# Kernel tuning notes

Hardware: AMD Instinct MI355X
Metric: run time of the kernel (lower is better)

The kernel has to match this reference:

```python
import jax, jax.numpy as jnp
import numpy as np

NUM_EMBEDDINGS = 1024
EMBEDDING_DIM = 256
COMMITMENT_COST = 0.25
DECAY = 0.99
EPS = 1e-5


def setup_inputs() -> dict:
    key = jax.random.key(0)
    k0, k1, k2 = jax.random.split(key, 3)
    x = jax.random.normal(k0, (32, 2048, EMBEDDING_DIM), dtype=jnp.float32)
    # embedding.weight.data.uniform_(-1/K, 1/K)
    embedding_w = jax.random.uniform(
        k1, (NUM_EMBEDDINGS, EMBEDDING_DIM), dtype=jnp.float32,
        minval=-1.0 / NUM_EMBEDDINGS, maxval=1.0 / NUM_EMBEDDINGS)
    ema_cluster_size = jnp.zeros((NUM_EMBEDDINGS,), dtype=jnp.float32)
    ema_w = jax.random.normal(k2, (NUM_EMBEDDINGS, EMBEDDING_DIM), dtype=jnp.float32)
    return {"x": x, "embedding_w": embedding_w,
            "ema_cluster_size": ema_cluster_size, "ema_w": ema_w}


def reference(x, embedding_w, ema_cluster_size, ema_w):
    K, D = embedding_w.shape
    flat = x.reshape(-1, D)  # [N, D]

    # squared L2 distances to codebook: [N, K]
    distances = ((flat * flat).sum(axis=1, keepdims=True)
                 - 2.0 * flat @ embedding_w.T
                 + (embedding_w * embedding_w).sum(axis=1))
    indices = jnp.argmin(distances, axis=1)  # [N] int

    # gather quantized vectors
    quantized = embedding_w[indices].reshape(x.shape)

    # EMA statistics via scatter-add (one-hot.T @ flat without materializing one-hot)
    counts = jax.ops.segment_sum(jnp.ones((flat.shape[0],), dtype=flat.dtype),
                                 indices, num_segments=K)  # [K]
    dw = jax.ops.segment_sum(flat, indices, num_segments=K)  # [K, D]

    new_cluster_size = DECAY * ema_cluster_size + (1.0 - DECAY) * counts
    new_ema_w = DECAY * ema_w + (1.0 - DECAY) * dw

    # Laplace smoothing of cluster sizes, normalized codebook update
    n = new_cluster_size.sum()
    cs = (new_cluster_size + EPS) / (n + K * EPS) * n
    new_embedding_w = new_ema_w / cs[:, None]

    # commitment loss (codebook side is EMA-updated, so only e-latent term)
    e_latent_loss = jnp.mean((jax.lax.stop_gradient(quantized) - x) ** 2)
    loss = COMMITMENT_COST * e_latent_loss

    # straight-through estimator
    quantized_st = x + jax.lax.stop_gradient(quantized - x)

    avg_probs = counts / counts.sum()
    perplexity = jnp.exp(-jnp.sum(avg_probs * jnp.log(avg_probs + 1e-10)))

    return (loss, quantized_st, perplexity,
            new_embedding_w, new_cluster_size, new_ema_w)
```

## Files before the change

kernel.cpp:

```cpp
#include <hip/hip_runtime.h>
#include <math.h>

#define N_ROWS   65536
#define K_EMB    1024
#define D_EMB    256

typedef __attribute__((ext_vector_type(8)))  short short8;
typedef __attribute__((ext_vector_type(4)))  short short4v;
typedef __attribute__((ext_vector_type(16))) float floatx16;

__device__ inline unsigned short f2bf(float f) {
    unsigned u = __float_as_uint(f);
    unsigned r = u + 0x7fffu + ((u >> 16) & 1u);
    return (unsigned short)(r >> 16);
}
__device__ inline float bf2f(unsigned short s) {
    return __uint_as_float(((unsigned)s) << 16);
}

__global__ __launch_bounds__(64)
void prep_e(const float* __restrict__ ew, float* __restrict__ half_esq,
            short* __restrict__ pack_hi, short* __restrict__ pack_lo,
            double* __restrict__ loss_buckets)
{
    const int k = blockIdx.x;
    const int t = threadIdx.x;

    if (t == 0 && k < 256) loss_buckets[k] = 0.0;

    float4 v = *(const float4*)(ew + (size_t)k * D_EMB + t * 4);
    float s = v.x * v.x + v.y * v.y + v.z * v.z + v.w * v.w;
#pragma unroll
    for (int off = 32; off > 0; off >>= 1) s += __shfl_down(s, off);
    if (t == 0) half_esq[k] = 0.5f * s;

    const int d0   = t * 4;
    const int tile = k >> 5;
    const int kt   = d0 >> 4;
    const int half = (d0 & 15) >> 3;
    const int lane = (k & 31) + 32 * half;
    const int j0   = d0 & 7;
    const int off  = tile * 8192 + kt * 512 + lane * 8 + j0;

    float f[4] = {-v.x, -v.y, -v.z, -v.w};
    short4v h, l;
#pragma unroll
    for (int j = 0; j < 4; ++j) {
        unsigned short hh = f2bf(f[j]);
        h[j] = (short)hh;
        l[j] = (short)f2bf(f[j] - bf2f(hh));
    }
    *(short4v*)(pack_hi + off) = h;
    *(short4v*)(pack_lo + off) = l;
}

__global__ __launch_bounds__(256, 2)
void argmin_mfma(const float* __restrict__ x,
                 const short* __restrict__ pack_hi,
                 const short* __restrict__ pack_lo,
                 const float* __restrict__ half_esq,
                 const float* __restrict__ ew,
                 int* __restrict__ indices,
                 float* __restrict__ out_q,
                 double* __restrict__ loss_buckets)
{
    __shared__ short xs_hi[32 * 256];
    __shared__ short xs_lo[32 * 256];
    __shared__ float cmv[128];
    __shared__ int   cmi[128];
    __shared__ int   widx[32];

    const int t  = threadIdx.x;
    const int r0 = blockIdx.x * 32;

#pragma unroll
    for (int i = 0; i < 4; ++i) {
        int q   = i * 256 + t;
        int row = q >> 5;
        int g8  = q & 31;
        const float* gp = x + (size_t)(r0 + row) * D_EMB + g8 * 8;
        float4 a = *(const float4*)gp;
        float4 b = *(const float4*)(gp + 4);
        float f[8] = {a.x, a.y, a.z, a.w, b.x, b.y, b.z, b.w};
        short8 h8, l8;
#pragma unroll
        for (int j = 0; j < 8; ++j) {
            unsigned short hh = f2bf(f[j]);
            h8[j] = (short)hh;
            l8[j] = (short)f2bf(f[j] - bf2f(hh));
        }
        int off = row * 256 + ((g8 ^ (row & 7)) << 3);
        *(short8*)(xs_hi + off) = h8;
        *(short8*)(xs_lo + off) = l8;
    }
    __syncthreads();

    const int w    = t >> 6;
    const int lane = t & 63;
    const int l31  = lane & 31;
    const int half = lane >> 5;
    const int key  = l31 & 7;
    const short* bbase_h = xs_hi + l31 * 256;
    const short* bbase_l = xs_lo + l31 * 256;

    float mv = 3.4e38f;
    int   mi = 0;

    for (int cp = 0; cp < 4; ++cp) {
        const int c0 = w * 256 + cp * 64;
        const int c1 = c0 + 32;
        const int tile0 = c0 >> 5;

        floatx16 acc0, acc1;
#pragma unroll
        for (int rq = 0; rq < 4; ++rq) {
            float4 e0 = *(const float4*)(half_esq + c0 + rq * 8 + half * 4);
            float4 e1 = *(const float4*)(half_esq + c1 + rq * 8 + half * 4);
            acc0[rq * 4 + 0] = e0.x; acc0[rq * 4 + 1] = e0.y;
            acc0[rq * 4 + 2] = e0.z; acc0[rq * 4 + 3] = e0.w;
            acc1[rq * 4 + 0] = e1.x; acc1[rq * 4 + 1] = e1.y;
            acc1[rq * 4 + 2] = e1.z; acc1[rq * 4 + 3] = e1.w;
        }

        const short* p0h = pack_hi + tile0 * 8192 + lane * 8;
        const short* p0l = pack_lo + tile0 * 8192 + lane * 8;
        const short* p1h = p0h + 8192;
        const short* p1l = p0l + 8192;

        short8 a0h = *(const short8*)(p0h);
        short8 a0l = *(const short8*)(p0l);
        short8 a1h = *(const short8*)(p1h);
        short8 a1l = *(const short8*)(p1l);

#pragma unroll 4
        for (int kt = 0; kt < 16; ++kt) {
            short8 n0h, n0l, n1h, n1l;
            if (kt < 15) {
                n0h = *(const short8*)(p0h + (kt + 1) * 512);
                n0l = *(const short8*)(p0l + (kt + 1) * 512);
                n1h = *(const short8*)(p1h + (kt + 1) * 512);
                n1l = *(const short8*)(p1l + (kt + 1) * 512);
            }
            int coff = (((2 * kt + half) ^ key) << 3);
            short8 bh = *(const short8*)(bbase_h + coff);
            short8 bl = *(const short8*)(bbase_l + coff);
            acc0 = __builtin_amdgcn_mfma_f32_32x32x16_bf16(a0h, bh, acc0, 0, 0, 0);
            acc1 = __builtin_amdgcn_mfma_f32_32x32x16_bf16(a1h, bh, acc1, 0, 0, 0);
            acc0 = __builtin_amdgcn_mfma_f32_32x32x16_bf16(a0h, bl, acc0, 0, 0, 0);
            acc1 = __builtin_amdgcn_mfma_f32_32x32x16_bf16(a1h, bl, acc1, 0, 0, 0);
            acc0 = __builtin_amdgcn_mfma_f32_32x32x16_bf16(a0l, bh, acc0, 0, 0, 0);
            acc1 = __builtin_amdgcn_mfma_f32_32x32x16_bf16(a1l, bh, acc1, 0, 0, 0);
            a0h = n0h; a0l = n0l; a1h = n1h; a1l = n1l;
        }

#pragma unroll
        for (int r = 0; r < 16; ++r) {
            int code0 = c0 + (r & 3) + ((r >> 2) << 3) + half * 4;
            float v0 = acc0[r];
            if (v0 < mv || (v0 == mv && code0 < mi)) { mv = v0; mi = code0; }
            int code1 = code0 + 32;
            float v1 = acc1[r];
            if (v1 < mv || (v1 == mv && code1 < mi)) { mv = v1; mi = code1; }
        }
    }

    {
        float ov = __shfl_xor(mv, 32);
        int   oi = __shfl_xor(mi, 32);
        if (ov < mv || (ov == mv && oi < mi)) { mv = ov; mi = oi; }
    }

    if (half == 0) {
        int slot = w * 32 + l31;
        cmv[slot] = mv;
        cmi[slot] = mi;
    }
    __syncthreads();
    if (t < 32) {
        float bv = cmv[t];
        int   bi = cmi[t];
#pragma unroll
        for (int ww = 1; ww < 4; ++ww) {
            float v = cmv[ww * 32 + t];
            int   i = cmi[ww * 32 + t];
            if (v < bv || (v == bv && i < bi)) { bv = v; bi = i; }
        }
        indices[r0 + t] = bi;
        widx[t] = bi;
    }
    __syncthreads();

    const int g8e  = lane >> 1;
    const int j0e  = (lane & 1) * 4;
    float lsum = 0.0f;
#pragma unroll
    for (int rr = 0; rr < 8; ++rr) {
        const int row = w * 8 + rr;
        const int idx = widx[row];
        const int off = row * 256 + (((g8e) ^ (row & 7)) << 3) + j0e;
        short4v h4 = *(const short4v*)(xs_hi + off);
        short4v l4 = *(const short4v*)(xs_lo + off);
        float xr[4];
#pragma unroll
        for (int j = 0; j < 4; ++j)
            xr[j] = bf2f((unsigned short)h4[j]) + bf2f((unsigned short)l4[j]);
        const float4 ev = *(const float4*)(ew + (size_t)idx * D_EMB + lane * 4);
        float4 q;
        q.x = xr[0] + (ev.x - xr[0]);
        q.y = xr[1] + (ev.y - xr[1]);
        q.z = xr[2] + (ev.z - xr[2]);
        q.w = xr[3] + (ev.w - xr[3]);
        *(float4*)(out_q + (size_t)(r0 + row) * D_EMB + lane * 4) = q;
        float dx = ev.x - xr[0], dy = ev.y - xr[1];
        float dz = ev.z - xr[2], dwv = ev.w - xr[3];
        lsum += dx * dx + dy * dy + dz * dz + dwv * dwv;
    }
#pragma unroll
    for (int off = 32; off > 0; off >>= 1) lsum += __shfl_down(lsum, off);
    if (lane == 0) atomicAdd(&loss_buckets[blockIdx.x & 255], (double)lsum);
}

__global__ __launch_bounds__(1024)
void finalize_small(const float* __restrict__ ema_cs,
                    const int* __restrict__ indices,
                    const double* __restrict__ loss_buckets,
                    float* __restrict__ cs_ws,
                    float* __restrict__ out_loss,
                    float* __restrict__ out_perp,
                    float* __restrict__ out_ncs,
                    int* __restrict__ counts,
                    int* __restrict__ offsets,
                    int* __restrict__ cursor)
{
    __shared__ int    hist[1024];
    __shared__ float  red[1024];
    __shared__ double redd[256];
    __shared__ int    sc[1024];
    const int k = threadIdx.x;

    hist[k] = 0;
    __syncthreads();
#pragma unroll
    for (int i = 0; i < 16; ++i) {
        int4 v = *(const int4*)(indices + (i * 1024 + k) * 4);
        atomicAdd(&hist[v.x], 1); atomicAdd(&hist[v.y], 1);
        atomicAdd(&hist[v.z], 1); atomicAdd(&hist[v.w], 1);
    }
    __syncthreads();

    const int icnt = hist[k];
    counts[k] = icnt;
    cursor[k] = 0;

    const float cnt = (float)icnt;
    const float ncs = 0.99f * ema_cs[k] + 0.01f * cnt;
    out_ncs[k] = ncs;
    red[k] = ncs;
    sc[k]  = icnt;
    __syncthreads();
    for (int off = 512; off > 0; off >>= 1) {
        if (k < off) red[k] += red[k + off];
        __syncthreads();
    }
    const float n = red[0];
    __syncthreads();
    cs_ws[k] = (ncs + 1e-5f) / (n + 1024.0f * 1e-5f) * n;

    for (int d = 1; d < 1024; d <<= 1) {
        int add = (k >= d) ? sc[k - d] : 0;
        __syncthreads();
        sc[k] += add;
        __syncthreads();
    }
    offsets[k] = sc[k] - icnt;

    const float p = cnt / 65536.0f;
    red[k] = p * logf(p + 1e-10f);
    if (k < 256) redd[k] = loss_buckets[k];
    __syncthreads();
    for (int off = 512; off > 0; off >>= 1) {
        if (k < off) red[k] += red[k + off];
        __syncthreads();
    }
    if (k == 0) out_perp[0] = expf(-red[0]);
    for (int off = 128; off > 0; off >>= 1) {
        if (k < off) redd[k] += redd[k + off];
        __syncthreads();
    }
    if (k == 0) out_loss[0] = (float)(0.25 * (redd[0] / 16777216.0));
}

__global__ __launch_bounds__(256)
void scatter_rows(const int* __restrict__ indices,
                  const int* __restrict__ offsets,
                  int* __restrict__ cursor,
                  int* __restrict__ row_sorted)
{
    const int row = blockIdx.x * 256 + threadIdx.x;
    const int idx = indices[row];
    const int pos = atomicAdd(&cursor[idx], 1);
    row_sorted[offsets[idx] + pos] = row;
}

__global__ __launch_bounds__(256)
void gather_update(const float* __restrict__ x,
                   const int* __restrict__ row_sorted,
                   const int* __restrict__ offsets,
                   const int* __restrict__ counts,
                   const float* __restrict__ ema_w,
                   const float* __restrict__ cs_ws,
                   float* __restrict__ out_emb,
                   float* __restrict__ out_ema)
{
    __shared__ int rows[2048];
    const int k   = blockIdx.x;
    const int t   = threadIdx.x;
    const int off = offsets[k];
    const int cnt = counts[k];
    float sum = 0.0f;

    for (int c = 0; c < cnt; c += 2048) {
        const int m = min(cnt - c, 2048);
        for (int i = t; i < m; i += 256) rows[i] = row_sorted[off + c + i];
        __syncthreads();
        int r = 0;
        for (; r + 4 <= m; r += 4) {
            int i0 = rows[r], i1 = rows[r + 1], i2 = rows[r + 2], i3 = rows[r + 3];
            float v0 = x[(size_t)i0 * D_EMB + t];
            float v1 = x[(size_t)i1 * D_EMB + t];
            float v2 = x[(size_t)i2 * D_EMB + t];
            float v3 = x[(size_t)i3 * D_EMB + t];
            sum += (v0 + v1) + (v2 + v3);
        }
        for (; r < m; ++r)
            sum += x[(size_t)rows[r] * D_EMB + t];
        __syncthreads();
    }

    const size_t o = (size_t)k * D_EMB + t;
    const float nev = 0.99f * ema_w[o] + 0.01f * sum;
    out_ema[o] = nev;
    out_emb[o] = nev / cs_ws[k];
}

extern "C" void kernel_launch(void* const* d_in, const int* in_sizes, int n_in,
                              void* d_out, int out_size, void* d_ws, size_t ws_size,
                              hipStream_t stream)
{
    const float* x       = (const float*)d_in[0];
    const float* ew      = (const float*)d_in[1];
    const float* ema_cs  = (const float*)d_in[2];
    const float* ema_w   = (const float*)d_in[3];

    float* out       = (float*)d_out;
    float* out_loss  = out;
    float* out_q     = out + 1;
    float* out_perp  = out + 1 + 16777216;
    float* out_emb   = out_perp + 1;
    float* out_ncs   = out_emb + 262144;
    float* out_ema   = out_ncs + 1024;

    char* ws = (char*)d_ws;
    int*    counts       = (int*)(ws);
    double* loss_buckets = (double*)(ws + 4096);
    float*  half_esq     = (float*)(ws + 6144);
    float*  cs_ws        = (float*)(ws + 10240);
    int*    offsets      = (int*)(ws + 14336);
    int*    cursor       = (int*)(ws + 18432);
    int*    indices      = (int*)(ws + 22528);
    int*    row_sorted   = (int*)(ws + 284672);

    short* pack_hi = (short*)(out + 16777220);
    short* pack_lo = (short*)(out + 16777220 + 131072);

    prep_e<<<K_EMB, 64, 0, stream>>>(ew, half_esq, pack_hi, pack_lo,
                                     loss_buckets);
    argmin_mfma<<<N_ROWS / 32, 256, 0, stream>>>(x, pack_hi, pack_lo, half_esq,
                                                 ew, indices, out_q, loss_buckets);
    finalize_small<<<1, 1024, 0, stream>>>(ema_cs, indices, loss_buckets, cs_ws,
                                           out_loss, out_perp, out_ncs,
                                           counts, offsets, cursor);
    scatter_rows<<<N_ROWS / 256, 256, 0, stream>>>(indices, offsets, cursor,
                                                   row_sorted);
    gather_update<<<K_EMB, 256, 0, stream>>>(x, row_sorted, offsets, counts,
                                             ema_w, cs_ws, out_emb, out_ema);
}
```

Measured before the change: 273.0 us.

## Fuse tail kernels into one cooperative kernel with grid syncs

Replaces the single-block finalize, scatter and gather kernels with one cooperative kernel of 512 blocks that uses grid-wide syncs between phases. The histogram is now built in parallel across 16 blocks with global atomics, so it no longer runs on a single workgroup, and two launches are removed. Each block now handles two codewords in the gather phase, which halves gather parallelism. The grid syncs and the cooperative launch add their own overhead.

```diff
diff --git a/kernel.cpp b/kernel.cpp
--- a/kernel.cpp
+++ b/kernel.cpp
@@ -1,5 +1,8 @@
 #include <hip/hip_runtime.h>
+#include <hip/hip_cooperative_groups.h>
 #include <math.h>
+
+namespace cg = cooperative_groups;
 
 #define N_ROWS   65536
 #define K_EMB    1024
@@ -21,12 +24,15 @@
 __global__ __launch_bounds__(64)
 void prep_e(const float* __restrict__ ew, float* __restrict__ half_esq,
             short* __restrict__ pack_hi, short* __restrict__ pack_lo,
-            double* __restrict__ loss_buckets)
+            int* __restrict__ counts, double* __restrict__ loss_buckets)
 {
     const int k = blockIdx.x;
     const int t = threadIdx.x;
 
-    if (t == 0 && k < 256) loss_buckets[k] = 0.0;
+    if (t == 0) {
+        counts[k] = 0;
+        if (k < 256) loss_buckets[k] = 0.0;
+    }
 
     float4 v = *(const float4*)(ew + (size_t)k * D_EMB + t * 4);
     float s = v.x * v.x + v.y * v.y + v.z * v.z + v.w * v.w;
@@ -220,127 +226,142 @@
     if (lane == 0) atomicAdd(&loss_buckets[blockIdx.x & 255], (double)lsum);
 }
 
-__global__ __launch_bounds__(1024)
-void finalize_small(const float* __restrict__ ema_cs,
-                    const int* __restrict__ indices,
-                    const double* __restrict__ loss_buckets,
-                    float* __restrict__ cs_ws,
-                    float* __restrict__ out_loss,
-                    float* __restrict__ out_perp,
-                    float* __restrict__ out_ncs,
-                    int* __restrict__ counts,
-                    int* __restrict__ offsets,
-                    int* __restrict__ cursor)
+__global__ __launch_bounds__(256, 4)
+void tail_update(const float* __restrict__ x,
+                 const int* __restrict__ indices,
+                 const float* __restrict__ ema_cs,
+                 const float* __restrict__ ema_w,
+                 const double* __restrict__ loss_buckets,
+                 int* __restrict__ counts,
+                 int* __restrict__ offsets,
+                 int* __restrict__ cursor,
+                 int* __restrict__ row_sorted,
+                 float* __restrict__ cs_ws,
+                 float* __restrict__ out_loss,
+                 float* __restrict__ out_perp,
+                 float* __restrict__ out_ncs,
+                 float* __restrict__ out_emb,
+                 float* __restrict__ out_ema)
 {
+    cg::grid_group grid = cg::this_grid();
     __shared__ int    hist[1024];
-    __shared__ float  red[1024];
-    __shared__ double redd[256];
-    __shared__ int    sc[1024];
-    const int k = threadIdx.x;
-
-    hist[k] = 0;
-    __syncthreads();
-#pragma unroll
-    for (int i = 0; i < 16; ++i) {
-        int4 v = *(const int4*)(indices + (i * 1024 + k) * 4);
-        atomicAdd(&hist[v.x], 1); atomicAdd(&hist[v.y], 1);
-        atomicAdd(&hist[v.z], 1); atomicAdd(&hist[v.w], 1);
-    }
-    __syncthreads();
-
-    const int icnt = hist[k];
-    counts[k] = icnt;
-    cursor[k] = 0;
-
-    const float cnt = (float)icnt;
-    const float ncs = 0.99f * ema_cs[k] + 0.01f * cnt;
-    out_ncs[k] = ncs;
-    red[k] = ncs;
-    sc[k]  = icnt;
-    __syncthreads();
-    for (int off = 512; off > 0; off >>= 1) {
-        if (k < off) red[k] += red[k + off];
+    __shared__ int    sci[256];
+    __shared__ float  scf[256];
+    __shared__ double scd[256];
+    __shared__ int    rows[2048];
+
+    const int t = threadIdx.x;
+    const int b = blockIdx.x;
+
+    if (b < 16) {
+#pragma unroll
+        for (int i = 0; i < 4; ++i) hist[i * 256 + t] = 0;
         __syncthreads();
-    }
-    const float n = red[0];
-    __syncthreads();
-    cs_ws[k] = (ncs + 1e-5f) / (n + 1024.0f * 1e-5f) * n;
-
-    for (int d = 1; d < 1024; d <<= 1) {
-        int add = (k >= d) ? sc[k - d] : 0;
+        const int base = b * 4096 + t * 16;
+#pragma unroll
+        for (int i = 0; i < 4; ++i) {
+            int4 v = *(const int4*)(indices + base + i * 4);
+            atomicAdd(&hist[v.x], 1); atomicAdd(&hist[v.y], 1);
+            atomicAdd(&hist[v.z], 1); atomicAdd(&hist[v.w], 1);
+        }
         __syncthreads();
-        sc[k] += add;
+#pragma unroll
+        for (int i = 0; i < 4; ++i) {
+            int c = hist[i * 256 + t];
+            if (c) atomicAdd(&counts[i * 256 + t], c);
+        }
+    }
+    grid.sync();
+
+    if (b == 0) {
+        int   c4[4];
+        float ncs4[4];
+        int   s = 0;
+        float npart = 0.0f;
+#pragma unroll
+        for (int j = 0; j < 4; ++j) {
+            const int k4 = t * 4 + j;
+            c4[j] = counts[k4];
+            s += c4[j];
+            ncs4[j] = 0.99f * ema_cs[k4] + 0.01f * (float)c4[j];
+            out_ncs[k4] = ncs4[j];
+            npart += ncs4[j];
+        }
+        sci[t] = s;
+        scf[t] = npart;
         __syncthreads();
-    }
-    offsets[k] = sc[k] - icnt;
-
-    const float p = cnt / 65536.0f;
-    red[k] = p * logf(p + 1e-10f);
-    if (k < 256) redd[k] = loss_buckets[k];
-    __syncthreads();
-    for (int off = 512; off > 0; off >>= 1) {
-        if (k < off) red[k] += red[k + off];
+        for (int d = 1; d < 256; d <<= 1) {
+            int add = (t >= d) ? sci[t - d] : 0;
+            __syncthreads();
+            sci[t] += add;
+            __syncthreads();
+        }
+        const int excl_base = sci[t] - s;
+        for (int off = 128; off > 0; off >>= 1) {
+            if (t < off) scf[t] += scf[t + off];
+            __syncthreads();
+        }
+        const float n = scf[0];
         __syncthreads();
-    }
-    if (k == 0) out_perp[0] = expf(-red[0]);
-    for (int off = 128; off > 0; off >>= 1) {
-        if (k < off) redd[k] += redd[k + off];
+        int run = excl_base;
+        float ppart = 0.0f;
+#pragma unroll
+        for (int j = 0; j < 4; ++j) {
+            const int k4 = t * 4 + j;
+            offsets[k4] = run; run += c4[j];
+            cursor[k4]  = 0;
+            cs_ws[k4] = (ncs4[j] + 1e-5f) / (n + 1024.0f * 1e-5f) * n;
+            const float p = (float)c4[j] / 65536.0f;
+            ppart += p * logf(p + 1e-10f);
+        }
+        scf[t] = ppart;
+        scd[t] = loss_buckets[t];
         __syncthreads();
-    }
-    if (k == 0) out_loss[0] = (float)(0.25 * (redd[0] / 16777216.0));
-}
-
-__global__ __launch_bounds__(256)
-void scatter_rows(const int* __restrict__ indices,
-                  const int* __restrict__ offsets,
-                  int* __restrict__ cursor,
-                  int* __restrict__ row_sorted)
-{
-    const int row = blockIdx.x * 256 + threadIdx.x;
-    const int idx = indices[row];
-    const int pos = atomicAdd(&cursor[idx], 1);
-    row_sorted[offsets[idx] + pos] = row;
-}
-
-__global__ __launch_bounds__(256)
-void gather_update(const float* __restrict__ x,
-                   const int* __restrict__ row_sorted,
-                   const int* __restrict__ offsets,
-                   const int* __restrict__ counts,
-                   const float* __restrict__ ema_w,
-                   const float* __restrict__ cs_ws,
-                   float* __restrict__ out_emb,
-                   float* __restrict__ out_ema)
-{
-    __shared__ int rows[2048];
-    const int k   = blockIdx.x;
-    const int t   = threadIdx.x;
-    const int off = offsets[k];
-    const int cnt = counts[k];
-    float sum = 0.0f;
-
-    for (int c = 0; c < cnt; c += 2048) {
-        const int m = min(cnt - c, 2048);
-        for (int i = t; i < m; i += 256) rows[i] = row_sorted[off + c + i];
-        __syncthreads();
-        int r = 0;
-        for (; r + 4 <= m; r += 4) {
-            int i0 = rows[r], i1 = rows[r + 1], i2 = rows[r + 2], i3 = rows[r + 3];
-            float v0 = x[(size_t)i0 * D_EMB + t];
-            float v1 = x[(size_t)i1 * D_EMB + t];
-            float v2 = x[(size_t)i2 * D_EMB + t];
-            float v3 = x[(size_t)i3 * D_EMB + t];
-            sum += (v0 + v1) + (v2 + v3);
-        }
-        for (; r < m; ++r)
-            sum += x[(size_t)rows[r] * D_EMB + t];
-        __syncthreads();
-    }
-
-    const size_t o = (size_t)k * D_EMB + t;
-    const float nev = 0.99f * ema_w[o] + 0.01f * sum;
-    out_ema[o] = nev;
-    out_emb[o] = nev / cs_ws[k];
+        for (int off = 128; off > 0; off >>= 1) {
+            if (t < off) { scf[t] += scf[t + off]; scd[t] += scd[t + off]; }
+            __syncthreads();
+        }
+        if (t == 0) {
+            out_perp[0] = expf(-scf[0]);
+            out_loss[0] = (float)(0.25 * (scd[0] / 16777216.0));
+        }
+    }
+    grid.sync();
+
+    if (t < 128) {
+        const int row = b * 128 + t;
+        const int idx = indices[row];
+        const int pos = atomicAdd(&cursor[idx], 1);
+        row_sorted[offsets[idx] + pos] = row;
+    }
+    grid.sync();
+
+    for (int kk = 2 * b; kk < 2 * b + 2; ++kk) {
+        const int off = offsets[kk];
+        const int cnt = counts[kk];
+        float sum = 0.0f;
+        for (int c = 0; c < cnt; c += 2048) {
+            const int m = min(cnt - c, 2048);
+            for (int i = t; i < m; i += 256) rows[i] = row_sorted[off + c + i];
+            __syncthreads();
+            int r = 0;
+            for (; r + 4 <= m; r += 4) {
+                int i0 = rows[r], i1 = rows[r + 1], i2 = rows[r + 2], i3 = rows[r + 3];
+                float v0 = x[(size_t)i0 * D_EMB + t];
+                float v1 = x[(size_t)i1 * D_EMB + t];
+                float v2 = x[(size_t)i2 * D_EMB + t];
+                float v3 = x[(size_t)i3 * D_EMB + t];
+                sum += (v0 + v1) + (v2 + v3);
+            }
+            for (; r < m; ++r)
+                sum += x[(size_t)rows[r] * D_EMB + t];
+            __syncthreads();
+        }
+        const size_t o = (size_t)kk * D_EMB + t;
+        const float nev = 0.99f * ema_w[o] + 0.01f * sum;
+        out_ema[o] = nev;
+        out_emb[o] = nev / cs_ws[kk];
+    }
 }
 
 extern "C" void kernel_launch(void* const* d_in, const int* in_sizes, int n_in,
@@ -374,14 +395,16 @@
     short* pack_lo = (short*)(out + 16777220 + 131072);
 
     prep_e<<<K_EMB, 64, 0, stream>>>(ew, half_esq, pack_hi, pack_lo,
-                                     loss_buckets);
+                                     counts, loss_buckets);
     argmin_mfma<<<N_ROWS / 32, 256, 0, stream>>>(x, pack_hi, pack_lo, half_esq,
                                                  ew, indices, out_q, loss_buckets);
-    finalize_small<<<1, 1024, 0, stream>>>(ema_cs, indices, loss_buckets, cs_ws,
-                                           out_loss, out_perp, out_ncs,
-                                           counts, offsets, cursor);
-    scatter_rows<<<N_ROWS / 256, 256, 0, stream>>>(indices, offsets, cursor,
-                                                   row_sorted);
-    gather_update<<<K_EMB, 256, 0, stream>>>(x, row_sorted, offsets, counts,
-                                             ema_w, cs_ws, out_emb, out_ema);
-}
+
+    void* args[] = {
+        (void*)&x, (void*)&indices, (void*)&ema_cs, (void*)&ema_w,
+        (void*)&loss_buckets, (void*)&counts, (void*)&offsets, (void*)&cursor,
+        (void*)&row_sorted, (void*)&cs_ws, (void*)&out_loss, (void*)&out_perp,
+        (void*)&out_ncs, (void*)&out_emb, (void*)&out_ema
+    };
+    hipLaunchCooperativeKernel((void*)tail_update, dim3(512), dim3(256),
+                               args, 0, stream);
+}
```

Result: slower. 430.2 us (+57.6%).
